# Kernel optimization log

Measured on AMD Instinct MI355X. Metric: run time of the kernel, lower is better.

The kernel has to match this reference:

```python
import jax, jax.numpy as jnp
import numpy as np

D_MODEL = 512
NUM_HEADS = 8
D_HEAD = 64
BATCH = 2
SEQ = 2048
NEG_BIG = 1.0e10


def setup_inputs() -> dict:
    key = jax.random.key(0)
    k1, k2, k3, k4, k5 = jax.random.split(key, 5)
    scale = D_MODEL ** -0.5
    return {
        "x": jax.random.normal(k1, (BATCH, SEQ, D_MODEL), dtype=jnp.float32),
        "W_Q": jax.random.normal(k2, (NUM_HEADS, D_HEAD, D_MODEL), dtype=jnp.float32) * scale,
        "W_K": jax.random.normal(k3, (NUM_HEADS, D_HEAD, D_MODEL), dtype=jnp.float32) * scale,
        "W_V": jax.random.normal(k4, (NUM_HEADS, D_HEAD, D_MODEL), dtype=jnp.float32) * scale,
        "W_O": jax.random.normal(k5, (D_MODEL, D_HEAD * NUM_HEADS), dtype=jnp.float32) * scale,
    }


def reference(x, W_Q, W_K, W_V, W_O):
    b, n, d = x.shape
    # q,k,v: [b, heads, pos, d_head]
    q = jnp.einsum('ihd,bpd->biph', W_Q, x)
    k = jnp.einsum('ihd,bpd->biph', W_K, x)
    v = jnp.einsum('ihd,bpd->biph', W_V, x)
    # scores: [b, heads, q_pos, k_pos]
    scores = jnp.einsum('biph,biqh->biqp', k, q)
    tril = jnp.tril(jnp.ones((n, n), dtype=scores.dtype))   # keep p <= q
    triu = jnp.triu(jnp.ones((n, n), dtype=scores.dtype))   # buffer 'mask'
    # Faithful to source: tril(scores) - 1e10 * (1 - triu)
    masked = scores * tril - NEG_BIG * (1.0 - triu)
    attn = jax.nn.softmax(masked / (D_HEAD ** 0.5), axis=-1)
    z = jnp.einsum('biph,biqp->biqh', v, attn)               # [b, i, q, h]
    z_flat = jnp.transpose(z, (0, 2, 1, 3)).reshape(b, n, -1)  # [b, q, i*h]
    out = jnp.einsum('df,bqf->bqd', W_O, z_flat)
    return out
```

## Files before the change

kernel.cpp:

```cpp
#include <hip/hip_runtime.h>
#include <stdint.h>

#define BATCH 2
#define SEQ 2048
#define DM 512
#define NH 8
#define DH 64
#define MROWS (BATCH * SEQ)
#define NCHUNK 64
#define CHUNK (SEQ / NCHUNK)

typedef __attribute__((ext_vector_type(8))) short bf16x8;
typedef __attribute__((ext_vector_type(4))) float f32x4;

__device__ __forceinline__ unsigned short f2bf(float f) {
    union { float f; uint32_t u; } x; x.f = f;
    uint32_t r = x.u + 0x7fffu + ((x.u >> 16) & 1u);
    return (unsigned short)(r >> 16);
}

__device__ __forceinline__ void gl_lds16(const void* g, void* l) {
    __builtin_amdgcn_global_load_lds(
        (const __attribute__((address_space(1))) void*)(uintptr_t)g,
        (__attribute__((address_space(3))) void*)(uint32_t)(uintptr_t)l,
        16, 0, 0);
}

__global__ void cvt_all(const float4* __restrict__ x,
                        const float* __restrict__ w0, const float* __restrict__ w1,
                        const float* __restrict__ w2, const float* __restrict__ w3,
                        ushort4* __restrict__ xb, ushort4* __restrict__ wb) {
    int i = blockIdx.x * blockDim.x + threadIdx.x;
    float4 v; ushort4* dst; int off;
    if (i < 524288) {
        v = x[i]; dst = xb; off = i;
    } else {
        int j = i - 524288;
        int wsel = j >> 16, wo = j & 65535;
        const float4* src = (const float4*)(wsel == 0 ? w0 : wsel == 1 ? w1 : wsel == 2 ? w2 : w3);
        v = src[wo]; dst = wb; off = j;
    }
    ushort4 o; o.x = f2bf(v.x); o.y = f2bf(v.y); o.z = f2bf(v.z); o.w = f2bf(v.w);
    dst[off] = o;
}

template<int TM, int TN, int WM, int WN>
__global__ __launch_bounds__(256) void gemm_bt(
    const unsigned short* __restrict__ A, const unsigned short* __restrict__ Bb,
    float* __restrict__ Cb, int M, int N, int K, int sBz, int sCz)
{
    constexpr int ROWS = TM + TN;
    constexpr int ROUNDS = ROWS / 64;
    constexpr int MI = WM / 16, NJ = WN / 16;
    constexpr int WAVES_N = TN / WN;
    const unsigned short* B = Bb + (size_t)blockIdx.z * sBz;
    float* C = Cb + (size_t)blockIdx.z * sCz;
    __shared__ __align__(16) unsigned short S[ROWS * 32];
    const int t = threadIdx.x, lane = t & 63, wave = t >> 6;
    const int wm = (wave / WAVES_N) * WM, wn = (wave % WAVES_N) * WN;
    const int m0 = blockIdx.x * TM, n0 = blockIdx.y * TN;
    const int lr = lane >> 2, lc = (lane & 3) * 8;

    const unsigned short* gbase[ROUNDS];
#pragma unroll
    for (int r = 0; r < ROUNDS; r++) {
        int grow = r * 64 + wave * 16 + lr;
        gbase[r] = (grow < TM) ? A + (size_t)(m0 + grow) * K + lc
                               : B + (size_t)(n0 + grow - TM) * K + lc;
    }

    f32x4 acc[MI][NJ];
#pragma unroll
    for (int i = 0; i < MI; i++)
#pragma unroll
        for (int j = 0; j < NJ; j++) { f32x4 z = {0.f, 0.f, 0.f, 0.f}; acc[i][j] = z; }

    const int mrow = wm + (lane & 15);
    const int nrow = TM + wn + (lane & 15);
    const int kcol = (lane >> 4) * 8;

    for (int k0 = 0; k0 < K; k0 += 32) {
        __syncthreads();
#pragma unroll
        for (int r = 0; r < ROUNDS; r++)
            gl_lds16(gbase[r] + k0, S + (r * 64 + wave * 16) * 32);
        __syncthreads();
        bf16x8 af[MI], bfr[NJ];
#pragma unroll
        for (int i = 0; i < MI; i++)
            af[i] = *(const bf16x8*)(S + (mrow + i * 16) * 32 + kcol);
#pragma unroll
        for (int j = 0; j < NJ; j++)
            bfr[j] = *(const bf16x8*)(S + (nrow + j * 16) * 32 + kcol);
#pragma unroll
        for (int i = 0; i < MI; i++)
#pragma unroll
            for (int j = 0; j < NJ; j++)
                acc[i][j] = __builtin_amdgcn_mfma_f32_16x16x32_bf16(af[i], bfr[j], acc[i][j], 0, 0, 0);
    }
    const int crow = m0 + wm + (lane >> 4) * 4;
    const int ccol = n0 + wn + (lane & 15);
#pragma unroll
    for (int i = 0; i < MI; i++)
#pragma unroll
        for (int j = 0; j < NJ; j++)
#pragma unroll
            for (int r = 0; r < 4; r++)
                C[(size_t)(crow + i * 16 + r) * N + ccol + j * 16] = acc[i][j][r];
}

__global__ __launch_bounds__(256) void coef_vsuf(
    const float* __restrict__ Q, const float* __restrict__ Kq,
    const float* __restrict__ V, float* __restrict__ cA, float* __restrict__ cW,
    float* __restrict__ csum) {
    int blk = blockIdx.x;
    if (blk < 128) {
        int idx = blk * 256 + threadIdx.x;
        int bp = idx >> 3, head = idx & 7;
        const float4* q = (const float4*)(Q + (size_t)bp * DM + head * DH);
        const float4* k = (const float4*)(Kq + (size_t)bp * DM + head * DH);
        float s = 0.f;
#pragma unroll
        for (int j = 0; j < 16; j++) {
            float4 a = q[j], b = k[j];
            s += a.x * b.x + a.y * b.y + a.z * b.z + a.w * b.w;
        }
        int p = bp & (SEQ - 1);
        float cnt = (float)(SEQ - 1 - p);
        float d = s * 0.125f;
        float M = fmaxf(d, 0.f);
        float a = expf(d - M);
        float e0 = expf(-M);
        float Z = a + cnt * e0;
        cA[idx] = a / Z;
        cW[idx] = e0 / Z;
    } else {
        int ci = (blk - 128) * 4 + (threadIdx.x >> 6);
        int h = threadIdx.x & 63;
        int c = ci & (NCHUNK - 1), bi = ci >> 6;
        int i = bi & 7, b = bi >> 3;
        const float* v = V + (size_t)(b * SEQ + c * CHUNK) * DM + i * DH + h;
        float s = 0.f;
#pragma unroll
        for (int j = 0; j < CHUNK; j++) s += v[(size_t)j * DM];
        csum[ci * 64 + h] = s;
    }
}

__global__ __launch_bounds__(256) void zbuild(
    const float* __restrict__ V, const float* __restrict__ csum,
    const float* __restrict__ cA, const float* __restrict__ cW,
    unsigned short* __restrict__ Zb) {
    int ci = blockIdx.x * 4 + (threadIdx.x >> 6);
    int h = threadIdx.x & 63;
    int c = ci & (NCHUNK - 1), bi = ci >> 6;
    int i = bi & 7, b = bi >> 3;
    float r = 0.f;
    for (int cc = c + 1; cc < NCHUNK; cc++) r += csum[((bi << 6) + cc) * 64 + h];
    for (int j = CHUNK - 1; j >= 0; j--) {
        int p = c * CHUNK + j;
        size_t row = (size_t)(b * SEQ + p);
        float v = V[row * DM + i * DH + h];
        float a = cA[row * NH + i], w = cW[row * NH + i];
        Zb[row * DM + i * DH + h] = f2bf(fmaf(a, v, w * r));
        r += v;
    }
}

extern "C" void kernel_launch(void* const* d_in, const int* in_sizes, int n_in,
                              void* d_out, int out_size, void* d_ws, size_t ws_size,
                              hipStream_t stream) {
    const float* x  = (const float*)d_in[0];
    const float* Wq = (const float*)d_in[1];
    const float* Wk = (const float*)d_in[2];
    const float* Wv = (const float*)d_in[3];
    const float* Wo = (const float*)d_in[4];
    float* out = (float*)d_out;
    char* ws = (char*)d_ws;

    unsigned short* xb = (unsigned short*)(ws);
    unsigned short* wb = (unsigned short*)(ws + 4194304);
    float* Q  = (float*)(ws + 6291456);
    float* Kp = (float*)(ws + 14680064);
    float* V  = (float*)(ws + 23068672);
    float* cA = (float*)(ws + 31457280);
    float* cW = (float*)(ws + 31588352);
    float* cs = (float*)(ws + 31719424);
    unsigned short* Zb = (unsigned short*)(ws + 31981568);

    cvt_all<<<3072, 256, 0, stream>>>((const float4*)x, Wq, Wk, Wv, Wo,
                                      (ushort4*)xb, (ushort4*)wb);
    gemm_bt<128, 64, 32, 64><<<dim3(32, 8, 3), 256, 0, stream>>>(
        xb, wb, Q, MROWS, DM, DM, 262144, 2097152);
    coef_vsuf<<<384, 256, 0, stream>>>(Q, Kp, V, cA, cW, cs);
    zbuild<<<256, 256, 0, stream>>>(V, cs, cA, cW, Zb);
    gemm_bt<64, 64, 32, 32><<<dim3(64, 8, 1), 256, 0, stream>>>(
        Zb, wb + 786432, out, MROWS, DM, DM, 0, 0);
}
```

Measured before the change: 116.6 us.

## Fuse QKV projection with diagonal-score coefficients and V chunk sums

Interleaves the W_Q and W_K rows per head during weight conversion so one GEMM tile yields both q and k for a head. The dot product and softmax coefficients are then computed in the epilogue, which avoids writing Q and K to memory. The V projection tile writes V as bf16 and computes the per-chunk column sums in its epilogue. This removes the separate coefficient/chunk-sum kernel and most fp32 intermediate traffic, at the cost of storing V in lower precision and a heavier per-block tile for the QK branch.

Measured after the change: 114.7 us (median of 2 runs). No clear change (-1.7%).

```diff
diff --git a/kernel.cpp b/kernel.cpp
--- a/kernel.cpp
+++ b/kernel.cpp
@@ -18,6 +18,10 @@
     uint32_t r = x.u + 0x7fffu + ((x.u >> 16) & 1u);
     return (unsigned short)(r >> 16);
 }
+__device__ __forceinline__ float bf2f(unsigned short s) {
+    union { uint32_t u; float f; } x; x.u = ((uint32_t)s) << 16;
+    return x.f;
+}
 
 __device__ __forceinline__ void gl_lds16(const void* g, void* l) {
     __builtin_amdgcn_global_load_lds(
@@ -27,8 +31,8 @@
 }
 
 __global__ void cvt_all(const float4* __restrict__ x,
-                        const float* __restrict__ w0, const float* __restrict__ w1,
-                        const float* __restrict__ w2, const float* __restrict__ w3,
+                        const float4* __restrict__ Wq, const float4* __restrict__ Wk,
+                        const float4* __restrict__ Wv, const float4* __restrict__ Wo,
                         ushort4* __restrict__ xb, ushort4* __restrict__ wb) {
     int i = blockIdx.x * blockDim.x + threadIdx.x;
     float4 v; ushort4* dst; int off;
@@ -36,119 +40,154 @@
         v = x[i]; dst = xb; off = i;
     } else {
         int j = i - 524288;
-        int wsel = j >> 16, wo = j & 65535;
-        const float4* src = (const float4*)(wsel == 0 ? w0 : wsel == 1 ? w1 : wsel == 2 ? w2 : w3);
-        v = src[wo]; dst = wb; off = j;
+        if (j < 131072) {
+            int head = j >> 14, rp = (j >> 7) & 127, colq = j & 127;
+            v = (rp < 64) ? Wq[head * 8192 + rp * 128 + colq]
+                          : Wk[head * 8192 + (rp - 64) * 128 + colq];
+        } else if (j < 196608) {
+            v = Wv[j - 131072];
+        } else {
+            v = Wo[j - 196608];
+        }
+        dst = wb; off = j;
     }
     ushort4 o; o.x = f2bf(v.x); o.y = f2bf(v.y); o.z = f2bf(v.z); o.w = f2bf(v.w);
     dst[off] = o;
 }
 
-template<int TM, int TN, int WM, int WN>
-__global__ __launch_bounds__(256) void gemm_bt(
-    const unsigned short* __restrict__ A, const unsigned short* __restrict__ Bb,
-    float* __restrict__ Cb, int M, int N, int K, int sBz, int sCz)
+__global__ __launch_bounds__(256) void proj(
+    const unsigned short* __restrict__ xb, const unsigned short* __restrict__ wb,
+    float* __restrict__ cA, float* __restrict__ cW,
+    unsigned short* __restrict__ V, float* __restrict__ csum)
 {
-    constexpr int ROWS = TM + TN;
-    constexpr int ROUNDS = ROWS / 64;
-    constexpr int MI = WM / 16, NJ = WN / 16;
-    constexpr int WAVES_N = TN / WN;
-    const unsigned short* B = Bb + (size_t)blockIdx.z * sBz;
-    float* C = Cb + (size_t)blockIdx.z * sCz;
-    __shared__ __align__(16) unsigned short S[ROWS * 32];
+    __shared__ __align__(16) unsigned short S[256 * 32];
     const int t = threadIdx.x, lane = t & 63, wave = t >> 6;
-    const int wm = (wave / WAVES_N) * WM, wn = (wave % WAVES_N) * WN;
-    const int m0 = blockIdx.x * TM, n0 = blockIdx.y * TN;
     const int lr = lane >> 2, lc = (lane & 3) * 8;
-
-    const unsigned short* gbase[ROUNDS];
-#pragma unroll
-    for (int r = 0; r < ROUNDS; r++) {
-        int grow = r * 64 + wave * 16 + lr;
-        gbase[r] = (grow < TM) ? A + (size_t)(m0 + grow) * K + lc
-                               : B + (size_t)(n0 + grow - TM) * K + lc;
-    }
-
-    f32x4 acc[MI][NJ];
-#pragma unroll
-    for (int i = 0; i < MI; i++)
-#pragma unroll
-        for (int j = 0; j < NJ; j++) { f32x4 z = {0.f, 0.f, 0.f, 0.f}; acc[i][j] = z; }
-
-    const int mrow = wm + (lane & 15);
-    const int nrow = TM + wn + (lane & 15);
+    const int bid = blockIdx.x;
+    const int wm = wave * 32;
     const int kcol = (lane >> 4) * 8;
-
-    for (int k0 = 0; k0 < K; k0 += 32) {
-        __syncthreads();
-#pragma unroll
-        for (int r = 0; r < ROUNDS; r++)
-            gl_lds16(gbase[r] + k0, S + (r * 64 + wave * 16) * 32);
-        __syncthreads();
-        bf16x8 af[MI], bfr[NJ];
-#pragma unroll
-        for (int i = 0; i < MI; i++)
-            af[i] = *(const bf16x8*)(S + (mrow + i * 16) * 32 + kcol);
-#pragma unroll
-        for (int j = 0; j < NJ; j++)
-            bfr[j] = *(const bf16x8*)(S + (nrow + j * 16) * 32 + kcol);
-#pragma unroll
-        for (int i = 0; i < MI; i++)
-#pragma unroll
-            for (int j = 0; j < NJ; j++)
-                acc[i][j] = __builtin_amdgcn_mfma_f32_16x16x32_bf16(af[i], bfr[j], acc[i][j], 0, 0, 0);
-    }
-    const int crow = m0 + wm + (lane >> 4) * 4;
-    const int ccol = n0 + wn + (lane & 15);
-#pragma unroll
-    for (int i = 0; i < MI; i++)
-#pragma unroll
-        for (int j = 0; j < NJ; j++)
+    const int l15 = lane & 15;
+
+    if (bid < 256) {
+        const int head = bid & 7, m0 = (bid >> 3) * 128;
+        const unsigned short* B = wb + head * 65536;
+        const unsigned short* gb[4];
+#pragma unroll
+        for (int r = 0; r < 4; r++) {
+            int grow = r * 64 + wave * 16 + lr;
+            gb[r] = (grow < 128) ? xb + (size_t)(m0 + grow) * 512 + lc
+                                 : B + (size_t)(grow - 128) * 512 + lc;
+        }
+        f32x4 acc[2][8];
+#pragma unroll
+        for (int i = 0; i < 2; i++)
+#pragma unroll
+            for (int j = 0; j < 8; j++) { f32x4 z = {0.f,0.f,0.f,0.f}; acc[i][j] = z; }
+        for (int k0 = 0; k0 < 512; k0 += 32) {
+            __syncthreads();
 #pragma unroll
             for (int r = 0; r < 4; r++)
-                C[(size_t)(crow + i * 16 + r) * N + ccol + j * 16] = acc[i][j][r];
-}
-
-__global__ __launch_bounds__(256) void coef_vsuf(
-    const float* __restrict__ Q, const float* __restrict__ Kq,
-    const float* __restrict__ V, float* __restrict__ cA, float* __restrict__ cW,
-    float* __restrict__ csum) {
-    int blk = blockIdx.x;
-    if (blk < 128) {
-        int idx = blk * 256 + threadIdx.x;
-        int bp = idx >> 3, head = idx & 7;
-        const float4* q = (const float4*)(Q + (size_t)bp * DM + head * DH);
-        const float4* k = (const float4*)(Kq + (size_t)bp * DM + head * DH);
-        float s = 0.f;
-#pragma unroll
-        for (int j = 0; j < 16; j++) {
-            float4 a = q[j], b = k[j];
-            s += a.x * b.x + a.y * b.y + a.z * b.z + a.w * b.w;
-        }
-        int p = bp & (SEQ - 1);
-        float cnt = (float)(SEQ - 1 - p);
-        float d = s * 0.125f;
-        float M = fmaxf(d, 0.f);
-        float a = expf(d - M);
-        float e0 = expf(-M);
-        float Z = a + cnt * e0;
-        cA[idx] = a / Z;
-        cW[idx] = e0 / Z;
+                gl_lds16(gb[r] + k0, S + (r * 64 + wave * 16) * 32);
+            __syncthreads();
+            bf16x8 af[2], bfr[8];
+#pragma unroll
+            for (int i = 0; i < 2; i++)
+                af[i] = *(const bf16x8*)(S + (wm + i * 16 + l15) * 32 + kcol);
+#pragma unroll
+            for (int j = 0; j < 8; j++)
+                bfr[j] = *(const bf16x8*)(S + (128 + j * 16 + l15) * 32 + kcol);
+#pragma unroll
+            for (int i = 0; i < 2; i++)
+#pragma unroll
+                for (int j = 0; j < 8; j++)
+                    acc[i][j] = __builtin_amdgcn_mfma_f32_16x16x32_bf16(af[i], bfr[j], acc[i][j], 0, 0, 0);
+        }
+#pragma unroll
+        for (int i = 0; i < 2; i++)
+#pragma unroll
+            for (int r = 0; r < 4; r++) {
+                float d = 0.f;
+#pragma unroll
+                for (int j = 0; j < 4; j++) d += acc[i][j][r] * acc[i][j + 4][r];
+                d += __shfl_xor(d, 1); d += __shfl_xor(d, 2);
+                d += __shfl_xor(d, 4); d += __shfl_xor(d, 8);
+                if (l15 == 0) {
+                    int row = m0 + wm + i * 16 + (lane >> 4) * 4 + r;
+                    int p = row & (SEQ - 1);
+                    float dd = d * 0.125f;
+                    float M = fmaxf(dd, 0.f);
+                    float a = expf(dd - M), e0 = expf(-M);
+                    float Z = a + (float)(SEQ - 1 - p) * e0;
+                    cA[row * NH + head] = a / Z;
+                    cW[row * NH + head] = e0 / Z;
+                }
+            }
     } else {
-        int ci = (blk - 128) * 4 + (threadIdx.x >> 6);
-        int h = threadIdx.x & 63;
-        int c = ci & (NCHUNK - 1), bi = ci >> 6;
-        int i = bi & 7, b = bi >> 3;
-        const float* v = V + (size_t)(b * SEQ + c * CHUNK) * DM + i * DH + h;
-        float s = 0.f;
-#pragma unroll
-        for (int j = 0; j < CHUNK; j++) s += v[(size_t)j * DM];
-        csum[ci * 64 + h] = s;
+        const int b2 = bid - 256;
+        const int head = b2 & 7, m0 = (b2 >> 3) * 128, n0 = head * 64;
+        const unsigned short* B = wb + 524288 + (size_t)n0 * 512;
+        const unsigned short* gb[3];
+#pragma unroll
+        for (int r = 0; r < 3; r++) {
+            int grow = r * 64 + wave * 16 + lr;
+            gb[r] = (grow < 128) ? xb + (size_t)(m0 + grow) * 512 + lc
+                                 : B + (size_t)(grow - 128) * 512 + lc;
+        }
+        f32x4 acc[2][4];
+#pragma unroll
+        for (int i = 0; i < 2; i++)
+#pragma unroll
+            for (int j = 0; j < 4; j++) { f32x4 z = {0.f,0.f,0.f,0.f}; acc[i][j] = z; }
+        for (int k0 = 0; k0 < 512; k0 += 32) {
+            __syncthreads();
+#pragma unroll
+            for (int r = 0; r < 3; r++)
+                gl_lds16(gb[r] + k0, S + (r * 64 + wave * 16) * 32);
+            __syncthreads();
+            bf16x8 af[2], bfr[4];
+#pragma unroll
+            for (int i = 0; i < 2; i++)
+                af[i] = *(const bf16x8*)(S + (wm + i * 16 + l15) * 32 + kcol);
+#pragma unroll
+            for (int j = 0; j < 4; j++)
+                bfr[j] = *(const bf16x8*)(S + (128 + j * 16 + l15) * 32 + kcol);
+#pragma unroll
+            for (int i = 0; i < 2; i++)
+#pragma unroll
+                for (int j = 0; j < 4; j++)
+                    acc[i][j] = __builtin_amdgcn_mfma_f32_16x16x32_bf16(af[i], bfr[j], acc[i][j], 0, 0, 0);
+        }
+        const int crow = m0 + wm + (lane >> 4) * 4;
+#pragma unroll
+        for (int i = 0; i < 2; i++)
+#pragma unroll
+            for (int j = 0; j < 4; j++)
+#pragma unroll
+                for (int r = 0; r < 4; r++)
+                    V[(size_t)(crow + i * 16 + r) * DM + n0 + j * 16 + l15] = f2bf(acc[i][j][r]);
+        float s[4];
+#pragma unroll
+        for (int j = 0; j < 4; j++) {
+            s[j] = 0.f;
+#pragma unroll
+            for (int i = 0; i < 2; i++)
+#pragma unroll
+                for (int r = 0; r < 4; r++) s[j] += acc[i][j][r];
+            s[j] += __shfl_xor(s[j], 16);
+            s[j] += __shfl_xor(s[j], 32);
+        }
+        if (lane < 16) {
+            int bi = (m0 >> 11) * NH + head;
+            int chunk = ((m0 & (SEQ - 1)) >> 5) + wave;
+#pragma unroll
+            for (int j = 0; j < 4; j++)
+                csum[(bi * NCHUNK + chunk) * 64 + j * 16 + lane] = s[j];
+        }
     }
 }
 
 __global__ __launch_bounds__(256) void zbuild(
-    const float* __restrict__ V, const float* __restrict__ csum,
+    const unsigned short* __restrict__ V, const float* __restrict__ csum,
     const float* __restrict__ cA, const float* __restrict__ cW,
     unsigned short* __restrict__ Zb) {
     int ci = blockIdx.x * 4 + (threadIdx.x >> 6);
@@ -160,11 +199,74 @@
     for (int j = CHUNK - 1; j >= 0; j--) {
         int p = c * CHUNK + j;
         size_t row = (size_t)(b * SEQ + p);
-        float v = V[row * DM + i * DH + h];
+        float v = bf2f(V[row * DM + i * DH + h]);
         float a = cA[row * NH + i], w = cW[row * NH + i];
         Zb[row * DM + i * DH + h] = f2bf(fmaf(a, v, w * r));
         r += v;
     }
+}
+
+template<int TM, int TN, int WM, int WN>
+__global__ __launch_bounds__(256) void gemm_bt(
+    const unsigned short* __restrict__ A, const unsigned short* __restrict__ B,
+    float* __restrict__ C, int M, int N, int K)
+{
+    constexpr int ROWS = TM + TN;
+    constexpr int ROUNDS = ROWS / 64;
+    constexpr int MI = WM / 16, NJ = WN / 16;
+    constexpr int WAVES_N = TN / WN;
+    __shared__ __align__(16) unsigned short S[ROWS * 32];
+    const int t = threadIdx.x, lane = t & 63, wave = t >> 6;
+    const int wm = (wave / WAVES_N) * WM, wn = (wave % WAVES_N) * WN;
+    const int m0 = blockIdx.x * TM, n0 = blockIdx.y * TN;
+    const int lr = lane >> 2, lc = (lane & 3) * 8;
+
+    const unsigned short* gbase[ROUNDS];
+#pragma unroll
+    for (int r = 0; r < ROUNDS; r++) {
+        int grow = r * 64 + wave * 16 + lr;
+        gbase[r] = (grow < TM) ? A + (size_t)(m0 + grow) * K + lc
+                               : B + (size_t)(n0 + grow - TM) * K + lc;
+    }
+
+    f32x4 acc[MI][NJ];
+#pragma unroll
+    for (int i = 0; i < MI; i++)
+#pragma unroll
+        for (int j = 0; j < NJ; j++) { f32x4 z = {0.f,0.f,0.f,0.f}; acc[i][j] = z; }
+
+    const int mrow = wm + (lane & 15);
+    const int nrow = TM + wn + (lane & 15);
+    const int kcol = (lane >> 4) * 8;
+
+    for (int k0 = 0; k0 < K; k0 += 32) {
+        __syncthreads();
+#pragma unroll
+        for (int r = 0; r < ROUNDS; r++)
+            gl_lds16(gbase[r] + k0, S + (r * 64 + wave * 16) * 32);
+        __syncthreads();
+        bf16x8 af[MI], bfr[NJ];
+#pragma unroll
+        for (int i = 0; i < MI; i++)
+            af[i] = *(const bf16x8*)(S + (mrow + i * 16) * 32 + kcol);
+#pragma unroll
+        for (int j = 0; j < NJ; j++)
+            bfr[j] = *(const bf16x8*)(S + (nrow + j * 16) * 32 + kcol);
+#pragma unroll
+        for (int i = 0; i < MI; i++)
+#pragma unroll
+            for (int j = 0; j < NJ; j++)
+                acc[i][j] = __builtin_amdgcn_mfma_f32_16x16x32_bf16(af[i], bfr[j], acc[i][j], 0, 0, 0);
+    }
+    const int crow = m0 + wm + (lane >> 4) * 4;
+    const int ccol = n0 + wn + (lane & 15);
+#pragma unroll
+    for (int i = 0; i < MI; i++)
+#pragma unroll
+        for (int j = 0; j < NJ; j++)
+#pragma unroll
+            for (int r = 0; r < 4; r++)
+                C[(size_t)(crow + i * 16 + r) * N + ccol + j * 16] = acc[i][j][r];
 }
 
 extern "C" void kernel_launch(void* const* d_in, const int* in_sizes, int n_in,
@@ -180,20 +282,17 @@
 
     unsigned short* xb = (unsigned short*)(ws);
     unsigned short* wb = (unsigned short*)(ws + 4194304);
-    float* Q  = (float*)(ws + 6291456);
-    float* Kp = (float*)(ws + 14680064);
-    float* V  = (float*)(ws + 23068672);
-    float* cA = (float*)(ws + 31457280);
-    float* cW = (float*)(ws + 31588352);
-    float* cs = (float*)(ws + 31719424);
-    unsigned short* Zb = (unsigned short*)(ws + 31981568);
-
-    cvt_all<<<3072, 256, 0, stream>>>((const float4*)x, Wq, Wk, Wv, Wo,
-                                      (ushort4*)xb, (ushort4*)wb);
-    gemm_bt<128, 64, 32, 64><<<dim3(32, 8, 3), 256, 0, stream>>>(
-        xb, wb, Q, MROWS, DM, DM, 262144, 2097152);
-    coef_vsuf<<<384, 256, 0, stream>>>(Q, Kp, V, cA, cW, cs);
+    unsigned short* V  = (unsigned short*)(ws + 6291456);
+    float* cA = (float*)(ws + 10485760);
+    float* cW = (float*)(ws + 10616832);
+    float* cs = (float*)(ws + 10747904);
+    unsigned short* Zb = (unsigned short*)(ws + 11010048);
+
+    cvt_all<<<3072, 256, 0, stream>>>((const float4*)x, (const float4*)Wq,
+                                      (const float4*)Wk, (const float4*)Wv,
+                                      (const float4*)Wo, (ushort4*)xb, (ushort4*)wb);
+    proj<<<512, 256, 0, stream>>>(xb, wb, cA, cW, V, cs);
     zbuild<<<256, 256, 0, stream>>>(V, cs, cA, cW, Zb);
     gemm_bt<64, 64, 32, 32><<<dim3(64, 8, 1), 256, 0, stream>>>(
-        Zb, wb + 786432, out, MROWS, DM, DM, 0, 0);
-}
+        Zb, wb + 786432, out, MROWS, DM, DM);
+}
```
